# Kernel tuning notes

Hardware: AMD Instinct MI355X
Metric: run time of the kernel (lower is better)

## Reference

```python
import jax, jax.numpy as jnp
import numpy as np

N = 100000          # total nodes in batch of junction trees
H = 256             # hidden_size
K = 8               # MAX_NUM_NEIGHBORS (padded neighbor slots)


def setup_inputs() -> dict:
    key = jax.random.key(0)
    k1, k2, k3, k4, k5, k6, k7 = jax.random.split(key, 7)
    scale = 1.0 / np.sqrt(H)
    inputs = {
        "prev_layer_output": jax.random.normal(k1, (N, H), dtype=jnp.float32),
        "W_U": jax.random.uniform(k2, (H, H), jnp.float32, -scale, scale),
        "W_V": jax.random.uniform(k3, (H, H), jnp.float32, -scale, scale),
        "W_A": jax.random.uniform(k4, (H, H), jnp.float32, -scale, scale),
        "W_B": jax.random.uniform(k5, (H, H), jnp.float32, -scale, scale),
        "parent_idxs": jnp.arange(N, dtype=jnp.int32),
        "child_idxs": jax.random.randint(k6, (N, K), 0, N, dtype=jnp.int32),
        "child_mask": jax.random.randint(k7, (N, K), 0, 2, dtype=jnp.int32).astype(jnp.bool_),
    }
    return inputs


def reference(prev_layer_output, W_U, W_V, W_A, W_B, parent_idxs, child_idxs, child_mask):
    # Gather parent hidden states: [E, H]
    ph = prev_layer_output[parent_idxs]
    # Gather child hidden states, zeroing padded slots (faithful to the
    # zero-vector padding in the original): [E, K, H]
    ch = jnp.where(child_mask[..., None], prev_layer_output[child_idxs], 0.0)

    # Edge gates: eta = sigmoid(A(parent)[:,None] + B(child)).
    # Padded slots still contribute sigmoid(A(parent)) — matches original.
    A_h = jnp.einsum('eh,ih->ei', ph, W_A)            # [E, H]
    B_h = jnp.einsum('ekh,ih->eki', ch, W_B)          # [E, K, H]
    eta = jax.nn.sigmoid(A_h[:, None, :] + B_h)       # [E, K, H]

    # Graph convolution: relu(U(parent) + sum_k (eta + V(child)))
    # NOTE: original ADDS eta to V_h (despite the 'mul' variable name).
    U_h = jnp.einsum('eh,ih->ei', ph, W_U)            # [E, H]
    V_h = jnp.einsum('ekh,ih->eki', ch, W_V)          # [E, K, H]
    new_h = jax.nn.relu(U_h + jnp.sum(eta + V_h, axis=1))  # [E, H]

    # Scatter into the current layer output (rows not updated stay zero).
    current = jnp.zeros_like(prev_layer_output).at[parent_idxs].set(new_h)
    return current
```

## Files before the change

### kernel.cpp

```cpp
#include <hip/hip_runtime.h>

#define HH 256
#define KK 8

typedef __attribute__((ext_vector_type(8))) short s16x8;
typedef __attribute__((ext_vector_type(4))) float f32x4;

__device__ __forceinline__ float bf2f(unsigned short u){ unsigned x=((unsigned)u)<<16; return __builtin_bit_cast(float,x); }
__device__ __forceinline__ unsigned short f2bf(float f){ unsigned x=__builtin_bit_cast(unsigned,f); return (unsigned short)((x+0x7fffu+((x>>16)&1u))>>16); }
__device__ __forceinline__ float sigmoidf(float x){ return __builtin_amdgcn_rcpf(1.0f + __expf(-x)); }

__global__ void cvt_bf16(const float* __restrict__ src, unsigned short* __restrict__ dst, int n8){
  int i = blockIdx.x*blockDim.x + threadIdx.x;
  if (i>=n8) return;
  const float4* s = reinterpret_cast<const float4*>(src);
  float4 a = s[i*2], b = s[i*2+1];
  uint4 o;
  o.x = (unsigned)f2bf(a.x) | ((unsigned)f2bf(a.y)<<16);
  o.y = (unsigned)f2bf(a.z) | ((unsigned)f2bf(a.w)<<16);
  o.z = (unsigned)f2bf(b.x) | ((unsigned)f2bf(b.y)<<16);
  o.w = (unsigned)f2bf(b.z) | ((unsigned)f2bf(b.w)<<16);
  reinterpret_cast<uint4*>(dst)[i] = o;
}

__global__ __launch_bounds__(512, 2)
void gemm_all(const float* __restrict__ prev,
              const unsigned short* __restrict__ wb,
              unsigned short* __restrict__ px,
              int n)
{
  __shared__ unsigned short As[128*HH];
  __shared__ unsigned short Bs[128*64];
  const int tid = threadIdx.x;
  const int m0  = blockIdx.x * 128;

  #pragma unroll
  for (int it=0; it<8; ++it){
    const int c = it*512 + tid;
    const int row = c>>5, kch = c&31;
    const int gm = m0 + row;
    uint4 o = {0u,0u,0u,0u};
    if (gm < n){
      const float4* sp = reinterpret_cast<const float4*>(prev + (size_t)gm*HH + kch*8);
      float4 f0 = sp[0], f1 = sp[1];
      o.x=(unsigned)f2bf(f0.x)|((unsigned)f2bf(f0.y)<<16);
      o.y=(unsigned)f2bf(f0.z)|((unsigned)f2bf(f0.w)<<16);
      o.z=(unsigned)f2bf(f1.x)|((unsigned)f2bf(f1.y)<<16);
      o.w=(unsigned)f2bf(f1.z)|((unsigned)f2bf(f1.w)<<16);
    }
    const int byte = row*512 + ((kch*16) ^ ((row&7)<<4));
    *reinterpret_cast<uint4*>(reinterpret_cast<char*>(As)+byte) = o;
  }

  const int lane=tid&63, wid=tid>>6;
  const int wr=wid>>1, wc=wid&1;
  const int lm=lane&15, kc=lane>>4;

  const int nn0 = tid>>3, kch0 = tid&7;
  const int bb0 = nn0*128 + ((kch0*16) ^ ((nn0&7)<<4));

  uint4 w0 = *reinterpret_cast<const uint4*>(wb + (size_t)nn0*HH + kch0*8);
  uint4 w1 = *reinterpret_cast<const uint4*>(wb + (size_t)(nn0+64)*HH + kch0*8);

  f32x4 acc[2][4];

  for (int step=0; step<32; ++step){
    const int g = step>>2, ks = step&3;
    __syncthreads();
    *reinterpret_cast<uint4*>(reinterpret_cast<char*>(Bs)+bb0)        = w0;
    *reinterpret_cast<uint4*>(reinterpret_cast<char*>(Bs)+bb0+8192)   = w1;
    __syncthreads();
    if (step < 31){
      const int s2 = step+1, g2 = s2>>2, ks2 = s2&3;
      const unsigned short* W = wb + (g2>>1)*65536 + (size_t)(g2&1)*128*HH + ks2*64;
      w0 = *reinterpret_cast<const uint4*>(W + (size_t)nn0*HH + kch0*8);
      w1 = *reinterpret_cast<const uint4*>(W + (size_t)(nn0+64)*HH + kch0*8);
    }
    if (ks==0){
      #pragma unroll
      for (int i=0;i<2;++i)
        #pragma unroll
        for (int j=0;j<4;++j) acc[i][j]=(f32x4){0.f,0.f,0.f,0.f};
    }
    #pragma unroll
    for (int kk=0; kk<2; ++kk){
      s16x8 af[2];
      #pragma unroll
      for (int i=0;i<2;++i){
        const int row = wr*32 + i*16 + lm;
        af[i] = *reinterpret_cast<const s16x8*>(reinterpret_cast<const char*>(As)
                  + row*512 + ((ks*128 + kk*64 + kc*16) ^ ((row&7)<<4)));
      }
      #pragma unroll
      for (int j=0; j<4; ++j){
        const int brow = wc*64 + j*16 + lm;
        s16x8 bf = *reinterpret_cast<const s16x8*>(reinterpret_cast<const char*>(Bs)
                  + brow*128 + ((kk*64 + kc*16) ^ ((brow&7)<<4)));
        #pragma unroll
        for (int i=0;i<2;++i)
          acc[i][j] = __builtin_amdgcn_mfma_f32_16x16x32_bf16(af[i], bf, acc[i][j], 0, 0, 0);
      }
    }
    if (ks==3){
      const int w_ = g>>1, h_ = g&1;
      #pragma unroll
      for (int i=0;i<2;++i){
        #pragma unroll
        for (int r=0;r<4;++r){
          const int gm = m0 + wr*32 + i*16 + kc*4 + r;
          if (gm < n){
            const size_t base = (size_t)gm*1024 + w_*256 + h_*128 + wc*64;
            #pragma unroll
            for (int j=0;j<4;++j)
              px[base + j*16 + lm] = f2bf(acc[i][j][r]);
          }
        }
      }
    }
  }
}

__global__ __launch_bounds__(256)
void epilogue(const unsigned short* __restrict__ px,
              const int* __restrict__ parent,
              const int* __restrict__ child,
              const int* __restrict__ mask,
              float* __restrict__ out,
              int n)
{
  const int e = blockIdx.x*8 + (threadIdx.x>>5);
  if (e >= n) return;
  const int c8 = (threadIdx.x & 31) * 8;
  const int p  = parent[e];

  const unsigned short* rp = px + (size_t)p*1024 + c8;
  uint4 av = *reinterpret_cast<const uint4*>(rp);
  uint4 uv = *reinterpret_cast<const uint4*>(rp + 256);
  const unsigned short* ap = reinterpret_cast<const unsigned short*>(&av);
  const unsigned short* up = reinterpret_cast<const unsigned short*>(&uv);

  float A[8], o[8], eta[8];
  #pragma unroll
  for (int j=0;j<8;++j){ A[j]=bf2f(ap[j]); o[j]=bf2f(up[j]); eta[j]=0.f; }

  int nm = 0;
  #pragma unroll
  for (int k=0;k<KK;++k){
    if (mask[(size_t)e*KK + k]){
      const unsigned short* rc = px + (size_t)child[(size_t)e*KK + k]*1024 + c8;
      uint4 pv = *reinterpret_cast<const uint4*>(rc + 512);
      uint4 pb = *reinterpret_cast<const uint4*>(rc + 768);
      const unsigned short* vp = reinterpret_cast<const unsigned short*>(&pv);
      const unsigned short* bp = reinterpret_cast<const unsigned short*>(&pb);
      #pragma unroll
      for (int j=0;j<8;++j){
        o[j]   += bf2f(vp[j]);
        eta[j] += sigmoidf(A[j] + bf2f(bp[j]));
      }
    } else ++nm;
  }

  const float fnm = (float)nm;
  #pragma unroll
  for (int j=0;j<8;++j){
    float s = o[j] + eta[j] + fnm * sigmoidf(A[j]);
    out[(size_t)p*HH + c8 + j] = s > 0.f ? s : 0.f;
  }
}

extern "C" void kernel_launch(void* const* d_in, const int* in_sizes, int n_in,
                              void* d_out, int out_size, void* d_ws, size_t ws_size,
                              hipStream_t stream)
{
  const float* prev = (const float*)d_in[0];
  const float* W_U  = (const float*)d_in[1];
  const float* W_V  = (const float*)d_in[2];
  const float* W_A  = (const float*)d_in[3];
  const float* W_B  = (const float*)d_in[4];
  const int* parent = (const int*)d_in[5];
  const int* child  = (const int*)d_in[6];
  const int* mask   = (const int*)d_in[7];
  float* out = (float*)d_out;

  const int n_nodes = in_sizes[5];

  unsigned short* wb = (unsigned short*)d_ws;
  unsigned short* px = wb + 4*65536;

  {
    const int w8 = 65536/8;
    cvt_bf16<<<(w8+255)/256, 256, 0, stream>>>(W_A, wb,           w8);
    cvt_bf16<<<(w8+255)/256, 256, 0, stream>>>(W_U, wb + 65536,   w8);
    cvt_bf16<<<(w8+255)/256, 256, 0, stream>>>(W_V, wb + 2*65536, w8);
    cvt_bf16<<<(w8+255)/256, 256, 0, stream>>>(W_B, wb + 3*65536, w8);
  }

  gemm_all<<<(n_nodes + 127)/128, 512, 0, stream>>>(prev, wb, px, n_nodes);

  epilogue<<<(n_nodes + 7)/8, 256, 0, stream>>>(px, parent, child, mask, out, n_nodes);
}
```

Baseline: 216.0 us.

## Stream weight panels via direct global-to-LDS loads and keep A fragments in registers

The GEMM now loads all A-operand fragments from LDS into registers once, then reuses the 64KB of shared memory as a double buffer for weight panels. The panels are filled with global_load_lds async copies instead of register-staged writes, and the loop is restructured into 8 output groups with two K-halves each. Launch bounds move to 4 waves per EU and the four weight conversion launches are merged into one. The aim is fewer barriers and LDS round trips per step and better overlap of weight loading with MFMA work. The cost is much higher register pressure from 16 A fragments per wave, and the swizzle in the direct-to-LDS copies must match the read pattern exactly.

```diff
diff --git a/kernel.cpp b/kernel.cpp
--- a/kernel.cpp
+++ b/kernel.cpp
@@ -5,14 +5,19 @@
 
 typedef __attribute__((ext_vector_type(8))) short s16x8;
 typedef __attribute__((ext_vector_type(4))) float f32x4;
+typedef __attribute__((address_space(3))) unsigned int lds_u32;
+typedef const __attribute__((address_space(1))) unsigned int glb_u32;
 
 __device__ __forceinline__ float bf2f(unsigned short u){ unsigned x=((unsigned)u)<<16; return __builtin_bit_cast(float,x); }
 __device__ __forceinline__ unsigned short f2bf(float f){ unsigned x=__builtin_bit_cast(unsigned,f); return (unsigned short)((x+0x7fffu+((x>>16)&1u))>>16); }
 __device__ __forceinline__ float sigmoidf(float x){ return __builtin_amdgcn_rcpf(1.0f + __expf(-x)); }
 
-__global__ void cvt_bf16(const float* __restrict__ src, unsigned short* __restrict__ dst, int n8){
-  int i = blockIdx.x*blockDim.x + threadIdx.x;
-  if (i>=n8) return;
+__global__ void cvt_w(const float* __restrict__ wa, const float* __restrict__ wu,
+                      const float* __restrict__ wv, const float* __restrict__ wbm,
+                      unsigned short* __restrict__ dst){
+  const int w = blockIdx.y;
+  const float* src = (w==0)? wa : (w==1)? wu : (w==2)? wv : wbm;
+  const int i = blockIdx.x*256 + threadIdx.x;
   const float4* s = reinterpret_cast<const float4*>(src);
   float4 a = s[i*2], b = s[i*2+1];
   uint4 o;
@@ -20,19 +25,21 @@
   o.y = (unsigned)f2bf(a.z) | ((unsigned)f2bf(a.w)<<16);
   o.z = (unsigned)f2bf(b.x) | ((unsigned)f2bf(b.y)<<16);
   o.w = (unsigned)f2bf(b.z) | ((unsigned)f2bf(b.w)<<16);
-  reinterpret_cast<uint4*>(dst)[i] = o;
-}
-
-__global__ __launch_bounds__(512, 2)
+  reinterpret_cast<uint4*>(dst + (size_t)w*65536)[i] = o;
+}
+
+__global__ __launch_bounds__(512, 4)
 void gemm_all(const float* __restrict__ prev,
               const unsigned short* __restrict__ wb,
               unsigned short* __restrict__ px,
               int n)
 {
-  __shared__ unsigned short As[128*HH];
-  __shared__ unsigned short Bs[128*64];
+  __shared__ char smem[65536];
   const int tid = threadIdx.x;
   const int m0  = blockIdx.x * 128;
+  const int lane = tid & 63, wid = tid >> 6;
+  const int wr = wid >> 1, wc = wid & 1;
+  const int lm = lane & 15, kc = lane >> 4;
 
   #pragma unroll
   for (int it=0; it<8; ++it){
@@ -48,76 +55,79 @@
       o.z=(unsigned)f2bf(f1.x)|((unsigned)f2bf(f1.y)<<16);
       o.w=(unsigned)f2bf(f1.z)|((unsigned)f2bf(f1.w)<<16);
     }
-    const int byte = row*512 + ((kch*16) ^ ((row&7)<<4));
-    *reinterpret_cast<uint4*>(reinterpret_cast<char*>(As)+byte) = o;
-  }
-
-  const int lane=tid&63, wid=tid>>6;
-  const int wr=wid>>1, wc=wid&1;
-  const int lm=lane&15, kc=lane>>4;
-
-  const int nn0 = tid>>3, kch0 = tid&7;
-  const int bb0 = nn0*128 + ((kch0*16) ^ ((nn0&7)<<4));
-
-  uint4 w0 = *reinterpret_cast<const uint4*>(wb + (size_t)nn0*HH + kch0*8);
-  uint4 w1 = *reinterpret_cast<const uint4*>(wb + (size_t)(nn0+64)*HH + kch0*8);
+    *reinterpret_cast<uint4*>(smem + row*512 + ((kch*16) ^ ((row&7)<<4))) = o;
+  }
+  __syncthreads();
+
+  s16x8 af[2][8];
+  #pragma unroll
+  for (int i=0;i<2;++i){
+    const int row = wr*32 + i*16 + lm;
+    #pragma unroll
+    for (int k8=0;k8<8;++k8)
+      af[i][k8] = *reinterpret_cast<const s16x8*>(smem + row*512 + ((k8*64 + kc*16) ^ ((row&7)<<4)));
+  }
+  __syncthreads();
+
+  const int rr = lane>>4, ks16 = (lane&15)*16;
+  const int off_e = rr*512 + (ks16 ^ (rr<<4));
+  const char* wbc = reinterpret_cast<const char*>(wb);
+
+  #define ISSUE_PANEL(Wp, lb)                                                      \
+    { _Pragma("unroll")                                                            \
+      for (int c_=0;c_<4;++c_){                                                    \
+        const int chunk_ = wid*4 + c_;                                             \
+        const char* ga_ = (Wp) + chunk_*2048 + ((c_&1)? (off_e^64) : off_e);       \
+        __builtin_amdgcn_global_load_lds((glb_u32*)ga_,                            \
+            (lds_u32*)((lb) + chunk_*1024), 16, 0, 0);                             \
+      } }
+
+  ISSUE_PANEL(wbc, smem)
 
   f32x4 acc[2][4];
-
-  for (int step=0; step<32; ++step){
-    const int g = step>>2, ks = step&3;
-    __syncthreads();
-    *reinterpret_cast<uint4*>(reinterpret_cast<char*>(Bs)+bb0)        = w0;
-    *reinterpret_cast<uint4*>(reinterpret_cast<char*>(Bs)+bb0+8192)   = w1;
-    __syncthreads();
-    if (step < 31){
-      const int s2 = step+1, g2 = s2>>2, ks2 = s2&3;
-      const unsigned short* W = wb + (g2>>1)*65536 + (size_t)(g2&1)*128*HH + ks2*64;
-      w0 = *reinterpret_cast<const uint4*>(W + (size_t)nn0*HH + kch0*8);
-      w1 = *reinterpret_cast<const uint4*>(W + (size_t)(nn0+64)*HH + kch0*8);
-    }
-    if (ks==0){
-      #pragma unroll
-      for (int i=0;i<2;++i)
-        #pragma unroll
-        for (int j=0;j<4;++j) acc[i][j]=(f32x4){0.f,0.f,0.f,0.f};
-    }
+  for (int g=0; g<8; ++g){
     #pragma unroll
-    for (int kk=0; kk<2; ++kk){
-      s16x8 af[2];
-      #pragma unroll
-      for (int i=0;i<2;++i){
-        const int row = wr*32 + i*16 + lm;
-        af[i] = *reinterpret_cast<const s16x8*>(reinterpret_cast<const char*>(As)
-                  + row*512 + ((ks*128 + kk*64 + kc*16) ^ ((row&7)<<4)));
-      }
-      #pragma unroll
-      for (int j=0; j<4; ++j){
-        const int brow = wc*64 + j*16 + lm;
-        s16x8 bf = *reinterpret_cast<const s16x8*>(reinterpret_cast<const char*>(Bs)
-                  + brow*128 + ((kk*64 + kc*16) ^ ((brow&7)<<4)));
+    for (int kh=0; kh<2; ++kh){
+      __syncthreads();
+      if (kh==0){
+        ISSUE_PANEL(wbc + g*65536 + 256, smem + 32768)
+      } else if (g < 7){
+        ISSUE_PANEL(wbc + (g+1)*65536, smem)
+      }
+      if (kh==0){
         #pragma unroll
         for (int i=0;i<2;++i)
-          acc[i][j] = __builtin_amdgcn_mfma_f32_16x16x32_bf16(af[i], bf, acc[i][j], 0, 0, 0);
-      }
-    }
-    if (ks==3){
-      const int w_ = g>>1, h_ = g&1;
+          #pragma unroll
+          for (int j=0;j<4;++j) acc[i][j]=(f32x4){0.f,0.f,0.f,0.f};
+      }
+      const char* rb = smem + kh*32768;
       #pragma unroll
-      for (int i=0;i<2;++i){
+      for (int kk=0; kk<4; ++kk){
         #pragma unroll
-        for (int r=0;r<4;++r){
-          const int gm = m0 + wr*32 + i*16 + kc*4 + r;
-          if (gm < n){
-            const size_t base = (size_t)gm*1024 + w_*256 + h_*128 + wc*64;
-            #pragma unroll
-            for (int j=0;j<4;++j)
-              px[base + j*16 + lm] = f2bf(acc[i][j][r]);
+        for (int j=0;j<4;++j){
+          const int brow = wc*64 + j*16 + lm;
+          s16x8 bf = *reinterpret_cast<const s16x8*>(rb + brow*256 + ((kk*64 + kc*16) ^ ((brow&7)<<4)));
+          acc[0][j] = __builtin_amdgcn_mfma_f32_16x16x32_bf16(af[0][kh*4+kk], bf, acc[0][j], 0, 0, 0);
+          acc[1][j] = __builtin_amdgcn_mfma_f32_16x16x32_bf16(af[1][kh*4+kk], bf, acc[1][j], 0, 0, 0);
+        }
+      }
+      if (kh==1){
+        #pragma unroll
+        for (int i=0;i<2;++i){
+          #pragma unroll
+          for (int r=0;r<4;++r){
+            const int gm = m0 + wr*32 + i*16 + kc*4 + r;
+            if (gm < n){
+              unsigned short* dp = px + (size_t)gm*1024 + g*128 + wc*64 + lm;
+              #pragma unroll
+              for (int j=0;j<4;++j) dp[j*16] = f2bf(acc[i][j][r]);
+            }
           }
         }
       }
     }
   }
+  #undef ISSUE_PANEL
 }
 
 __global__ __launch_bounds__(256)
@@ -187,13 +197,8 @@
   unsigned short* wb = (unsigned short*)d_ws;
   unsigned short* px = wb + 4*65536;
 
-  {
-    const int w8 = 65536/8;
-    cvt_bf16<<<(w8+255)/256, 256, 0, stream>>>(W_A, wb,           w8);
-    cvt_bf16<<<(w8+255)/256, 256, 0, stream>>>(W_U, wb + 65536,   w8);
-    cvt_bf16<<<(w8+255)/256, 256, 0, stream>>>(W_V, wb + 2*65536, w8);
-    cvt_bf16<<<(w8+255)/256, 256, 0, stream>>>(W_B, wb + 3*65536, w8);
-  }
+  dim3 gc(32, 4);
+  cvt_w<<<gc, 256, 0, stream>>>(W_A, W_U, W_V, W_B, wb);
 
   gemm_all<<<(n_nodes + 127)/128, 512, 0, stream>>>(prev, wb, px, n_nodes);
 
```

New measurement: 225.1 us. 1.04x slower.
